# Performance work log

Measured on AMD Instinct MI355X. Metric: run time of the kernel, lower is better.

The kernel has to match this reference:

```python
import jax, jax.numpy as jnp
import numpy as np

BN_EPS = 1e-5

def batch_norm(x, gamma, beta):
    # training-mode BatchNorm1d: biased batch stats over the edge dim
    mean = jnp.mean(x, axis=0)
    var = jnp.var(x, axis=0)
    return (x - mean) * jax.lax.rsqrt(var + BN_EPS) * gamma + beta

def setup_inputs() -> dict:
    key = jax.random.key(0)
    ks = jax.random.split(key, 10)
    N, F, E = 50000, 128, 600000
    D_in = 2 * F + 12  # 268
    h = jax.random.normal(ks[0], (N, F), dtype=jnp.float32)
    edge_feature = jax.random.normal(ks[1], (E, 12), dtype=jnp.float32)
    src = jax.random.randint(ks[2], (E,), 0, N)
    dst = jax.random.randint(ks[3], (E,), 0, N)
    def lin(k, fan_in, shape):
        bound = 1.0 / np.sqrt(fan_in)
        return jax.random.uniform(k, shape, jnp.float32, -bound, bound)
    W1 = lin(ks[4], D_in, (28, D_in)); b1 = lin(ks[5], D_in, (28,))
    W2 = lin(ks[6], 28, (8, 28));      b2 = lin(ks[7], 28, (8,))
    W3 = lin(ks[8], 8, (1, 8));        b3 = lin(ks[9], 8, (1,))
    gamma1 = jnp.ones((28,), jnp.float32); beta1 = jnp.zeros((28,), jnp.float32)
    gamma2 = jnp.ones((8,), jnp.float32);  beta2 = jnp.zeros((8,), jnp.float32)
    return {"h": h, "edge_feature": edge_feature, "src": src, "dst": dst,
            "W1": W1, "b1": b1, "gamma1": gamma1, "beta1": beta1,
            "W2": W2, "b2": b2, "gamma2": gamma2, "beta2": beta2,
            "W3": W3, "b3": b3}

def reference(h, edge_feature, src, dst, W1, b1, gamma1, beta1,
              W2, b2, gamma2, beta2, W3, b3):
    h_u = h[src]                    # [E, F] gather of source node feats
    h_v = h[dst]                    # [E, F] gather of dest node feats
    x = jnp.concatenate([h_u, h_v, edge_feature], axis=1)  # [E, 2F+12]
    s = jax.nn.relu(batch_norm(x @ W1.T + b1, gamma1, beta1))  # [E, 28]
    s = jax.nn.relu(batch_norm(s @ W2.T + b2, gamma2, beta2))  # [E, 8]
    score = s @ W3.T + b3           # [E, 1]
    return score
```

## Files before the change

kernel.cpp:

```cpp
#include <hip/hip_runtime.h>

#define BN_EPS 1e-5f
typedef unsigned short u16;
typedef unsigned int u32;


__device__ __forceinline__ u16 f2bf(float f) {
  u32 u = __float_as_uint(f);
  return (u16)((u + 0x7fffu + ((u >> 16) & 1u)) >> 16);
}
__device__ __forceinline__ float bf2f(u16 s) {
  return __uint_as_float(((u32)s) << 16);
}
__device__ __forceinline__ u32 pack2(float a, float b) {
  return (u32)f2bf(a) | ((u32)f2bf(b) << 16);
}

__global__ void k1_proj(const float* __restrict__ h, const float* __restrict__ W1,
                        u16* __restrict__ Psrc, u16* __restrict__ Pdst,
                        float* __restrict__ stats, int N) {
  if (blockIdx.x == 0 && threadIdx.x < 72) stats[threadIdx.x] = 0.f;
  const int half = blockIdx.x & 1;
  const int node = (blockIdx.x >> 1) * 256 + threadIdx.x;
  if (node >= N) return;
  const float* __restrict__ wbase = W1 + half * 128;
  const float4* __restrict__ h4 = (const float4*)(h + (size_t)node * 128);
  float acc[28];
#pragma unroll
  for (int c = 0; c < 28; c++) acc[c] = 0.f;
  for (int kk = 0; kk < 16; kk++) {
    const float4 a = h4[kk * 2];
    const float4 b = h4[kk * 2 + 1];
#pragma unroll
    for (int c = 0; c < 28; c++) {
      const float* w = wbase + c * 268 + kk * 8;
      acc[c] += a.x * w[0] + a.y * w[1] + a.z * w[2] + a.w * w[3]
              + b.x * w[4] + b.y * w[5] + b.z * w[6] + b.w * w[7];
    }
  }
  u16* out = (half == 0 ? Psrc : Pdst) + (size_t)node * 32;
  u32 u[14];
#pragma unroll
  for (int j = 0; j < 14; j++) u[j] = pack2(acc[2 * j], acc[2 * j + 1]);
  uint4* p4 = (uint4*)out;
  p4[0] = make_uint4(u[0], u[1], u[2], u[3]);
  p4[1] = make_uint4(u[4], u[5], u[6], u[7]);
  p4[2] = make_uint4(u[8], u[9], u[10], u[11]);
  *(uint2*)((u32*)out + 12) = make_uint2(u[12], u[13]);
}

__global__ void k2_l1(const u16* __restrict__ Psrc, const u16* __restrict__ Pdst,
                      const float* __restrict__ ef,
                      const int* __restrict__ src, const int* __restrict__ dst,
                      const float* __restrict__ W1, const float* __restrict__ b1,
                      u16* __restrict__ y1, float* __restrict__ stats, int E) {
  const int tid = threadIdx.x;
  const int c = tid & 31;
  const int g = tid >> 5;
  const bool act = (c < 28);
  float w[12];
  float bias = 0.f;
  if (act) {
    const float4* wp = (const float4*)(W1 + c * 268 + 256);
    float4 w0 = wp[0], w1 = wp[1], w2 = wp[2];
    w[0] = w0.x; w[1] = w0.y; w[2] = w0.z; w[3] = w0.w;
    w[4] = w1.x; w[5] = w1.y; w[6] = w1.z; w[7] = w1.w;
    w[8] = w2.x; w[9] = w2.y; w[10] = w2.z; w[11] = w2.w;
    bias = b1[c];
  }
  float sum = 0.f, ssq = 0.f;
  const int gstride = gridDim.x * 8;
  for (int e = blockIdx.x * 8 + g; e < E; e += gstride) {
    const int s = src[e], d = dst[e];
    if (act) {
      const float pa = bf2f(Psrc[(size_t)s * 32 + c]);
      const float pb = bf2f(Pdst[(size_t)d * 32 + c]);
      const float4* e4 = (const float4*)(ef + (size_t)e * 12);
      float4 f0 = e4[0], f1 = e4[1], f2 = e4[2];
      const float y = bias
          + f0.x * w[0] + f0.y * w[1] + f0.z * w[2] + f0.w * w[3]
          + f1.x * w[4] + f1.y * w[5] + f1.z * w[6] + f1.w * w[7]
          + f2.x * w[8] + f2.y * w[9] + f2.z * w[10] + f2.w * w[11]
          + pa + pb;
      y1[(size_t)e * 32 + c] = f2bf(y);
      sum += y;
      ssq += y * y;
    }
  }
  sum += __shfl_xor(sum, 32);
  ssq += __shfl_xor(ssq, 32);
  __shared__ float red[2][4][28];
  const int wave = tid >> 6, lane = tid & 63;
  if (lane < 28) { red[0][wave][lane] = sum; red[1][wave][lane] = ssq; }
  __syncthreads();
  if (tid < 28) {
    atomicAdd(&stats[tid], red[0][0][tid] + red[0][1][tid] + red[0][2][tid] + red[0][3][tid]);
    atomicAdd(&stats[28 + tid], red[1][0][tid] + red[1][1][tid] + red[1][2][tid] + red[1][3][tid]);
  }
}

__global__ void k4_l2(const u16* __restrict__ y1, const float* __restrict__ stats,
                      const float* __restrict__ g1, const float* __restrict__ be1,
                      const float* __restrict__ W2, const float* __restrict__ b2,
                      u16* __restrict__ y2, float* __restrict__ stats2, int E, float invE) {
  float sc[28], sh[28];
#pragma unroll
  for (int cc = 0; cc < 28; cc++) {
    const float m = stats[cc] * invE;
    const float v = stats[28 + cc] * invE - m * m;
    const float s = g1[cc] * rsqrtf(v + BN_EPS);
    sc[cc] = s; sh[cc] = be1[cc] - m * s;
  }
  float as[8], aq[8];
#pragma unroll
  for (int o = 0; o < 8; o++) { as[o] = 0.f; aq[o] = 0.f; }
  const int stride = gridDim.x * blockDim.x;
  for (int e = blockIdx.x * blockDim.x + threadIdx.x; e < E; e += stride) {
    const u16* row = y1 + (size_t)e * 32;
    const uint4 r0 = *(const uint4*)row;
    const uint4 r1 = *(const uint4*)(row + 8);
    const uint4 r2 = *(const uint4*)(row + 16);
    const uint2 r3 = *(const uint2*)(row + 24);
    u32 uu[14] = {r0.x, r0.y, r0.z, r0.w, r1.x, r1.y, r1.z, r1.w,
                  r2.x, r2.y, r2.z, r2.w, r3.x, r3.y};
    float acc[8];
#pragma unroll
    for (int o = 0; o < 8; o++) acc[o] = b2[o];
#pragma unroll
    for (int k = 0; k < 14; k++) {
      const float fe = __uint_as_float(uu[k] << 16);
      const float fo = __uint_as_float(uu[k] & 0xffff0000u);
      const float se = fmaxf(fmaf(fe, sc[2 * k], sh[2 * k]), 0.f);
      const float so = fmaxf(fmaf(fo, sc[2 * k + 1], sh[2 * k + 1]), 0.f);
#pragma unroll
      for (int o = 0; o < 8; o++) {
        acc[o] = fmaf(W2[o * 28 + 2 * k], se, acc[o]);
        acc[o] = fmaf(W2[o * 28 + 2 * k + 1], so, acc[o]);
      }
    }
    *(uint4*)(y2 + (size_t)e * 8) = make_uint4(pack2(acc[0], acc[1]), pack2(acc[2], acc[3]),
                                               pack2(acc[4], acc[5]), pack2(acc[6], acc[7]));
#pragma unroll
    for (int o = 0; o < 8; o++) { as[o] += acc[o]; aq[o] += acc[o] * acc[o]; }
  }
#pragma unroll
  for (int o = 0; o < 8; o++) {
    for (int off = 32; off; off >>= 1) {
      as[o] += __shfl_down(as[o], off);
      aq[o] += __shfl_down(aq[o], off);
    }
  }
  __shared__ float redS[4][16];
  const int wave = threadIdx.x >> 6, lane = threadIdx.x & 63;
  if (lane == 0) {
#pragma unroll
    for (int o = 0; o < 8; o++) { redS[wave][o] = as[o]; redS[wave][8 + o] = aq[o]; }
  }
  __syncthreads();
  if (threadIdx.x < 16) {
    const int t = threadIdx.x;
    atomicAdd(&stats2[t], redS[0][t] + redS[1][t] + redS[2][t] + redS[3][t]);
  }
}

__global__ void k6_l3(const u16* __restrict__ y2, const float* __restrict__ stats,
                      const float* __restrict__ g2, const float* __restrict__ be2,
                      const float* __restrict__ W3, const float* __restrict__ b3,
                      float* __restrict__ out, int E, float invE) {
  float sc[8], sh[8], w3[8];
#pragma unroll
  for (int o = 0; o < 8; o++) {
    const float m = stats[56 + o] * invE;
    const float v = stats[64 + o] * invE - m * m;
    const float s = g2[o] * rsqrtf(v + BN_EPS);
    sc[o] = s; sh[o] = be2[o] - m * s; w3[o] = W3[o];
  }
  const int e = blockIdx.x * blockDim.x + threadIdx.x;
  if (e >= E) return;
  const uint4 r = *(const uint4*)(y2 + (size_t)e * 8);
  u32 uu[4] = {r.x, r.y, r.z, r.w};
  float acc = b3[0];
#pragma unroll
  for (int k = 0; k < 4; k++) {
    const float fe = __uint_as_float(uu[k] << 16);
    const float fo = __uint_as_float(uu[k] & 0xffff0000u);
    acc = fmaf(w3[2 * k], fmaxf(fmaf(fe, sc[2 * k], sh[2 * k]), 0.f), acc);
    acc = fmaf(w3[2 * k + 1], fmaxf(fmaf(fo, sc[2 * k + 1], sh[2 * k + 1]), 0.f), acc);
  }
  out[e] = acc;
}

extern "C" void kernel_launch(void* const* d_in, const int* in_sizes, int n_in,
                              void* d_out, int out_size, void* d_ws, size_t ws_size,
                              hipStream_t stream) {
  const float* h   = (const float*)d_in[0];
  const float* ef  = (const float*)d_in[1];
  const int* src   = (const int*)d_in[2];
  const int* dst   = (const int*)d_in[3];
  const float* W1  = (const float*)d_in[4];
  const float* b1  = (const float*)d_in[5];
  const float* g1  = (const float*)d_in[6];
  const float* be1 = (const float*)d_in[7];
  const float* W2  = (const float*)d_in[8];
  const float* b2  = (const float*)d_in[9];
  const float* g2  = (const float*)d_in[10];
  const float* be2 = (const float*)d_in[11];
  const float* W3  = (const float*)d_in[12];
  const float* b3  = (const float*)d_in[13];
  float* out = (float*)d_out;

  const int N = in_sizes[0] / 128;
  const int E = in_sizes[2];
  const float invE = 1.0f / (float)E;

  char* ws = (char*)d_ws;
  float* stats = (float*)ws;
  u16* Psrc = (u16*)(ws + 1024);
  u16* Pdst = Psrc + (size_t)N * 32;
  u16* y1   = Pdst + (size_t)N * 32;
  u16* y2   = y1 + (size_t)E * 32;

  const int nodeBlocks = (N + 255) / 256;
  k1_proj<<<nodeBlocks * 2, 256, 0, stream>>>(h, W1, Psrc, Pdst, stats, N);
  k2_l1<<<2560, 256, 0, stream>>>(Psrc, Pdst, ef, src, dst, W1, b1, y1, stats, E);
  k4_l2<<<1172, 256, 0, stream>>>(y1, stats, g1, be1, W2, b2, y2, stats + 56, E, invE);
  k6_l3<<<(E + 255) / 256, 256, 0, stream>>>(y2, stats, g2, be2, W3, b3, out, E, invE);
}
```

Measured before the change: 310.2 us.

## Restructure edge-layer gathers per wave and stage layer-2 rows through LDS

k2_l1 now gives each wave a contiguous range of edges and processes four edges at a time. The lower half-wave gathers from Psrc and the upper half from Pdst, and the two halves are combined with a cross-half shuffle. Output stores are nontemporal. k4_l2 loads y1 tiles coalesced into padded shared memory before per-thread compute, launches one block per 256 edges, and loads y1 nontemporally. The aim is more memory-level parallelism and coalesced access, at the cost of extra LDS traffic, syncs and redundant edge-feature loads across lanes.

```diff
diff --git a/kernel.cpp b/kernel.cpp
--- a/kernel.cpp
+++ b/kernel.cpp
@@ -38,60 +38,105 @@
               + b.x * w[4] + b.y * w[5] + b.z * w[6] + b.w * w[7];
     }
   }
-  u16* out = (half == 0 ? Psrc : Pdst) + (size_t)node * 32;
+  u16* outp = (half == 0 ? Psrc : Pdst) + (size_t)node * 32;
   u32 u[14];
 #pragma unroll
   for (int j = 0; j < 14; j++) u[j] = pack2(acc[2 * j], acc[2 * j + 1]);
-  uint4* p4 = (uint4*)out;
+  uint4* p4 = (uint4*)outp;
   p4[0] = make_uint4(u[0], u[1], u[2], u[3]);
   p4[1] = make_uint4(u[4], u[5], u[6], u[7]);
   p4[2] = make_uint4(u[8], u[9], u[10], u[11]);
-  *(uint2*)((u32*)out + 12) = make_uint2(u[12], u[13]);
-}
-
-__global__ void k2_l1(const u16* __restrict__ Psrc, const u16* __restrict__ Pdst,
-                      const float* __restrict__ ef,
-                      const int* __restrict__ src, const int* __restrict__ dst,
-                      const float* __restrict__ W1, const float* __restrict__ b1,
-                      u16* __restrict__ y1, float* __restrict__ stats, int E) {
+  *(uint2*)((u32*)outp + 12) = make_uint2(u[12], u[13]);
+}
+
+__global__ void __launch_bounds__(256) k2_l1(
+    const u16* __restrict__ Psrc, const u16* __restrict__ Pdst,
+    const float* __restrict__ ef,
+    const int* __restrict__ src, const int* __restrict__ dst,
+    const float* __restrict__ W1, const float* __restrict__ b1,
+    u16* __restrict__ y1, float* __restrict__ stats, int E, int epw) {
   const int tid = threadIdx.x;
-  const int c = tid & 31;
-  const int g = tid >> 5;
-  const bool act = (c < 28);
+  const int lane = tid & 63;
+  const int c = lane & 31;
+  const int wv = __builtin_amdgcn_readfirstlane(tid >> 6);
+  const int wid = blockIdx.x * 4 + wv;
+  int e0 = wid * epw;
+  int e1 = e0 + epw;
+  if (e1 > E) e1 = E;
+  if (e0 > e1) e0 = e1;
+
+  const bool isA = (lane < 28);
   float w[12];
+#pragma unroll
+  for (int j = 0; j < 12; j++) w[j] = 0.f;
   float bias = 0.f;
-  if (act) {
-    const float4* wp = (const float4*)(W1 + c * 268 + 256);
+  if (isA) {
+    const float4* wp = (const float4*)(W1 + lane * 268 + 256);
     float4 w0 = wp[0], w1 = wp[1], w2 = wp[2];
     w[0] = w0.x; w[1] = w0.y; w[2] = w0.z; w[3] = w0.w;
     w[4] = w1.x; w[5] = w1.y; w[6] = w1.z; w[7] = w1.w;
     w[8] = w2.x; w[9] = w2.y; w[10] = w2.z; w[11] = w2.w;
-    bias = b1[c];
-  }
+    bias = b1[lane];
+  }
+
   float sum = 0.f, ssq = 0.f;
-  const int gstride = gridDim.x * 8;
-  for (int e = blockIdx.x * 8 + g; e < E; e += gstride) {
-    const int s = src[e], d = dst[e];
-    if (act) {
-      const float pa = bf2f(Psrc[(size_t)s * 32 + c]);
-      const float pb = bf2f(Pdst[(size_t)d * 32 + c]);
-      const float4* e4 = (const float4*)(ef + (size_t)e * 12);
-      float4 f0 = e4[0], f1 = e4[1], f2 = e4[2];
-      const float y = bias
-          + f0.x * w[0] + f0.y * w[1] + f0.z * w[2] + f0.w * w[3]
-          + f1.x * w[4] + f1.y * w[5] + f1.z * w[6] + f1.w * w[7]
-          + f2.x * w[8] + f2.y * w[9] + f2.z * w[10] + f2.w * w[11]
-          + pa + pb;
-      y1[(size_t)e * 32 + c] = f2bf(y);
+  int e = e0;
+  for (; e + 4 <= e1; e += 4) {
+    int sI[4], dI[4];
+#pragma unroll
+    for (int k = 0; k < 4; k++) { sI[k] = src[e + k]; dI[k] = dst[e + k]; }
+    float efv[4][12];
+#pragma unroll
+    for (int k = 0; k < 4; k++) {
+      const float* er = ef + (size_t)(e + k) * 12;
+#pragma unroll
+      for (int j = 0; j < 12; j++) efv[k][j] = er[j];
+    }
+    float p[4];
+    if (lane < 32) {
+#pragma unroll
+      for (int k = 0; k < 4; k++) p[k] = bf2f(Psrc[(size_t)(u32)sI[k] * 32 + c]);
+    } else {
+#pragma unroll
+      for (int k = 0; k < 4; k++) p[k] = bf2f(Pdst[(size_t)(u32)dI[k] * 32 + c]);
+    }
+#pragma unroll
+    for (int k = 0; k < 4; k++) {
+      float part = bias;
+#pragma unroll
+      for (int j = 0; j < 12; j++) part = fmaf(efv[k][j], w[j], part);
+      part += p[k];
+      const float y = part + __shfl_xor(part, 32);
+      if (isA) {
+        sum += y;
+        ssq += y * y;
+        __builtin_nontemporal_store(f2bf(y), &y1[(size_t)(e + k) * 32 + (u32)lane]);
+      }
+    }
+  }
+  for (; e < e1; e++) {
+    const int sI = src[e], dI = dst[e];
+    float efv[12];
+    const float* er = ef + (size_t)e * 12;
+#pragma unroll
+    for (int j = 0; j < 12; j++) efv[j] = er[j];
+    float p;
+    if (lane < 32) p = bf2f(Psrc[(size_t)(u32)sI * 32 + c]);
+    else           p = bf2f(Pdst[(size_t)(u32)dI * 32 + c]);
+    float part = bias;
+#pragma unroll
+    for (int j = 0; j < 12; j++) part = fmaf(efv[j], w[j], part);
+    part += p;
+    const float y = part + __shfl_xor(part, 32);
+    if (isA) {
       sum += y;
       ssq += y * y;
-    }
-  }
-  sum += __shfl_xor(sum, 32);
-  ssq += __shfl_xor(ssq, 32);
+      __builtin_nontemporal_store(f2bf(y), &y1[(size_t)e * 32 + (u32)lane]);
+    }
+  }
+
   __shared__ float red[2][4][28];
-  const int wave = tid >> 6, lane = tid & 63;
-  if (lane < 28) { red[0][wave][lane] = sum; red[1][wave][lane] = ssq; }
+  if (lane < 28) { red[0][wv][lane] = sum; red[1][wv][lane] = ssq; }
   __syncthreads();
   if (tid < 28) {
     atomicAdd(&stats[tid], red[0][0][tid] + red[0][1][tid] + red[0][2][tid] + red[0][3][tid]);
@@ -99,10 +144,12 @@
   }
 }
 
-__global__ void k4_l2(const u16* __restrict__ y1, const float* __restrict__ stats,
-                      const float* __restrict__ g1, const float* __restrict__ be1,
-                      const float* __restrict__ W2, const float* __restrict__ b2,
-                      u16* __restrict__ y2, float* __restrict__ stats2, int E, float invE) {
+__global__ void __launch_bounds__(256) k4_l2(
+    const u32* __restrict__ y1w, const float* __restrict__ stats,
+    const float* __restrict__ g1, const float* __restrict__ be1,
+    const float* __restrict__ W2, const float* __restrict__ b2,
+    u16* __restrict__ y2, float* __restrict__ stats2, int E, float invE) {
+  __shared__ u32 tile[256 * 17];
   float sc[28], sh[28];
 #pragma unroll
   for (int cc = 0; cc < 28; cc++) {
@@ -114,34 +161,41 @@
   float as[8], aq[8];
 #pragma unroll
   for (int o = 0; o < 8; o++) { as[o] = 0.f; aq[o] = 0.f; }
-  const int stride = gridDim.x * blockDim.x;
-  for (int e = blockIdx.x * blockDim.x + threadIdx.x; e < E; e += stride) {
-    const u16* row = y1 + (size_t)e * 32;
-    const uint4 r0 = *(const uint4*)row;
-    const uint4 r1 = *(const uint4*)(row + 8);
-    const uint4 r2 = *(const uint4*)(row + 16);
-    const uint2 r3 = *(const uint2*)(row + 24);
-    u32 uu[14] = {r0.x, r0.y, r0.z, r0.w, r1.x, r1.y, r1.z, r1.w,
-                  r2.x, r2.y, r2.z, r2.w, r3.x, r3.y};
-    float acc[8];
-#pragma unroll
-    for (int o = 0; o < 8; o++) acc[o] = b2[o];
-#pragma unroll
-    for (int k = 0; k < 14; k++) {
-      const float fe = __uint_as_float(uu[k] << 16);
-      const float fo = __uint_as_float(uu[k] & 0xffff0000u);
-      const float se = fmaxf(fmaf(fe, sc[2 * k], sh[2 * k]), 0.f);
-      const float so = fmaxf(fmaf(fo, sc[2 * k + 1], sh[2 * k + 1]), 0.f);
-#pragma unroll
-      for (int o = 0; o < 8; o++) {
-        acc[o] = fmaf(W2[o * 28 + 2 * k], se, acc[o]);
-        acc[o] = fmaf(W2[o * 28 + 2 * k + 1], so, acc[o]);
+  const int tid = threadIdx.x;
+  for (int T = blockIdx.x * 256; T < E; T += gridDim.x * 256) {
+    int cnt = E - T; if (cnt > 256) cnt = 256;
+    __syncthreads();
+    const int total = cnt * 16;
+    for (int i = tid; i < total; i += 256) {
+      tile[(i >> 4) * 17 + (i & 15)] =
+          __builtin_nontemporal_load(&y1w[(size_t)T * 16 + i]);
+    }
+    __syncthreads();
+    if (tid < cnt) {
+      u32 uu[14];
+#pragma unroll
+      for (int i = 0; i < 14; i++) uu[i] = tile[tid * 17 + i];
+      float acc[8];
+#pragma unroll
+      for (int o = 0; o < 8; o++) acc[o] = b2[o];
+#pragma unroll
+      for (int k = 0; k < 14; k++) {
+        const float fe = __uint_as_float(uu[k] << 16);
+        const float fo = __uint_as_float(uu[k] & 0xffff0000u);
+        const float se = fmaxf(fmaf(fe, sc[2 * k], sh[2 * k]), 0.f);
+        const float so = fmaxf(fmaf(fo, sc[2 * k + 1], sh[2 * k + 1]), 0.f);
+#pragma unroll
+        for (int o = 0; o < 8; o++) {
+          acc[o] = fmaf(W2[o * 28 + 2 * k], se, acc[o]);
+          acc[o] = fmaf(W2[o * 28 + 2 * k + 1], so, acc[o]);
+        }
       }
-    }
-    *(uint4*)(y2 + (size_t)e * 8) = make_uint4(pack2(acc[0], acc[1]), pack2(acc[2], acc[3]),
-                                               pack2(acc[4], acc[5]), pack2(acc[6], acc[7]));
-#pragma unroll
-    for (int o = 0; o < 8; o++) { as[o] += acc[o]; aq[o] += acc[o] * acc[o]; }
+      *(uint4*)(y2 + (size_t)(T + tid) * 8) =
+          make_uint4(pack2(acc[0], acc[1]), pack2(acc[2], acc[3]),
+                     pack2(acc[4], acc[5]), pack2(acc[6], acc[7]));
+#pragma unroll
+      for (int o = 0; o < 8; o++) { as[o] += acc[o]; aq[o] += acc[o] * acc[o]; }
+    }
   }
 #pragma unroll
   for (int o = 0; o < 8; o++) {
@@ -151,15 +205,14 @@
     }
   }
   __shared__ float redS[4][16];
-  const int wave = threadIdx.x >> 6, lane = threadIdx.x & 63;
+  const int wave = tid >> 6, lane = tid & 63;
   if (lane == 0) {
 #pragma unroll
     for (int o = 0; o < 8; o++) { redS[wave][o] = as[o]; redS[wave][8 + o] = aq[o]; }
   }
   __syncthreads();
-  if (threadIdx.x < 16) {
-    const int t = threadIdx.x;
-    atomicAdd(&stats2[t], redS[0][t] + redS[1][t] + redS[2][t] + redS[3][t]);
+  if (tid < 16) {
+    atomicAdd(&stats2[tid], redS[0][tid] + redS[1][tid] + redS[2][tid] + redS[3][tid]);
   }
 }
 
@@ -222,7 +275,13 @@
 
   const int nodeBlocks = (N + 255) / 256;
   k1_proj<<<nodeBlocks * 2, 256, 0, stream>>>(h, W1, Psrc, Pdst, stats, N);
-  k2_l1<<<2560, 256, 0, stream>>>(Psrc, Pdst, ef, src, dst, W1, b1, y1, stats, E);
-  k4_l2<<<1172, 256, 0, stream>>>(y1, stats, g1, be1, W2, b2, y2, stats + 56, E, invE);
+
+  const int K2B = 2560;
+  const int epw = (E + K2B * 4 - 1) / (K2B * 4);
+  k2_l1<<<K2B, 256, 0, stream>>>(Psrc, Pdst, ef, src, dst, W1, b1, y1, stats, E, epw);
+
+  const int K4B = (E + 255) / 256;
+  k4_l2<<<K4B, 256, 0, stream>>>((const u32*)y1, stats, g1, be1, W2, b2, y2,
+                                 stats + 56, E, invE);
   k6_l3<<<(E + 255) / 256, 256, 0, stream>>>(y2, stats, g2, be2, W3, b3, out, E, invE);
 }
```

Measured after the change: 330.2 us. 6.4% more time.
